# Kernel tuning notes

Hardware: AMD Instinct MI355X
Metric: run time of the kernel (lower is better)

## Reference

```python
import jax, jax.numpy as jnp
import numpy as np

U10_IDX, V10_IDX = 0, 1
WIND_THRESH = 0.5


def _gru(x, h, Wih, Whh, bih, bhh):
    # standard torch GRUCell math
    gi = x @ Wih.T + bih
    gh = h @ Whh.T + bhh
    ir, iz, inn = jnp.split(gi, 3, axis=-1)
    hr, hz, hnn = jnp.split(gh, 3, axis=-1)
    r = jax.nn.sigmoid(ir + hr)
    z = jax.nn.sigmoid(iz + hz)
    n = jnp.tanh(inn + r * hnn)
    return (1.0 - z) * n + z * h


def setup_inputs() -> dict:
    B, N, H, F, Th, Tf = 256, 184, 128, 8, 24, 24
    key = jax.random.key(0)
    ks = jax.random.split(key, 24)
    s = 0.1
    f32 = jnp.float32
    feature = jax.random.normal(ks[0], (B, Th + Tf, N, F), f32)
    pm25_hist = jax.random.uniform(ks[1], (B, Th, N, 1), dtype=f32)
    adj_mat = (jax.random.uniform(ks[2], (N, N)) < 0.1).astype(f32)
    angles = jax.random.uniform(ks[3], (N, N), f32, 0.0, 2.0 * np.pi)
    C = F + 1  # ChebConv in-channels = in_dim + out_dim
    return dict(
        feature=feature, pm25_hist=pm25_hist, adj_mat=adj_mat, angles=angles,
        W_ih_hist=s * jax.random.normal(ks[4], (3 * H, 2), f32),
        W_hh_hist=s * jax.random.normal(ks[5], (3 * H, H), f32),
        b_ih_hist=s * jax.random.normal(ks[6], (3 * H,), f32),
        b_hh_hist=s * jax.random.normal(ks[7], (3 * H,), f32),
        fc_hist_w=s * jax.random.normal(ks[8], (1, H), f32),
        fc_hist_b=s * jax.random.normal(ks[9], (1,), f32),
        cheb_w0=s * jax.random.normal(ks[10], (C, 1), f32),
        cheb_w1=s * jax.random.normal(ks[11], (C, 1), f32),
        cheb_b=s * jax.random.normal(ks[12], (1,), f32),
        W_ih=s * jax.random.normal(ks[13], (3 * H, C + 1), f32),
        W_hh=s * jax.random.normal(ks[14], (3 * H, H), f32),
        b_ih=s * jax.random.normal(ks[15], (3 * H,), f32),
        b_hh=s * jax.random.normal(ks[16], (3 * H,), f32),
        fc_out_w=s * jax.random.normal(ks[17], (1, H), f32),
        fc_out_b=s * jax.random.normal(ks[18], (1,), f32),
    )


def reference(feature, pm25_hist, adj_mat, angles,
              W_ih_hist, W_hh_hist, b_ih_hist, b_hh_hist,
              fc_hist_w, fc_hist_b,
              cheb_w0, cheb_w1, cheb_b,
              W_ih, W_hh, b_ih, b_hh,
              fc_out_w, fc_out_b):
    B, T, N, F = feature.shape
    H = W_hh.shape[1]
    Th = pm25_hist.shape[1]
    comp1 = jnp.cos(angles)                                # [N,N]
    comp2 = jnp.cos(angles - jnp.float32(np.pi / 2.0))     # [N,N]
    adj_b = adj_mat > 0

    # ---- history GRU over pm25_hist ----
    def hist_step(carry, p):
        hn, xn = carry
        x = jnp.concatenate([xn, p], axis=-1).reshape(B * N, 2)
        hn = _gru(x, hn, W_ih_hist, W_hh_hist, b_ih_hist, b_hh_hist)
        xn = hn.reshape(B, N, H) @ fc_hist_w.T + fc_hist_b
        return (hn, xn), None

    h0 = jnp.zeros((B * N, H), feature.dtype)
    x0 = jnp.zeros((B, N, 1), feature.dtype)
    (hn, xn), _ = jax.lax.scan(hist_step, (h0, x0), jnp.swapaxes(pm25_hist, 0, 1))

    # ---- forecast: dynamic wind-gated graph + ChebConv(K=2) + GRU ----
    def fore_step(carry, f):
        hn, xn = carry
        x = jnp.concatenate([xn, f], axis=-1)              # [B,N,F+1]
        u = f[..., U10_IDX]                                # [B,N]
        v = f[..., V10_IDX]
        wind = u[:, :, None] * comp1[None] + v[:, :, None] * comp2[None]
        # edge i->j iff adj and wind projection >= threshold
        M = jnp.logical_and(wind >= WIND_THRESH, adj_b[None]).astype(x.dtype)
        deg = M.sum(-1)                                    # source degree [B,N]
        has = deg > 0
        dinv = jnp.where(has, 1.0 / jnp.sqrt(jnp.where(has, deg, 1.0)), 0.0)
        # ChebConv scaled Laplacian (lambda_max=2, sym norm):
        # L_hat x [j] = -dinv_j * sum_i dinv_i * M[i,j] * x[i] + (0 if deg_j>0 else -1) * x[j]
        y = jnp.einsum('bij,bic->bjc', M * dinv[:, :, None], x)
        y = -dinv[:, :, None] * y + jnp.where(has, 0.0, -1.0)[:, :, None] * x
        g = jax.nn.sigmoid(x @ cheb_w0 + y @ cheb_w1 + cheb_b)  # [B,N,1]
        x2 = jnp.concatenate([x, g], axis=-1).reshape(B * N, F + 2)
        hn = _gru(x2, hn, W_ih, W_hh, b_ih, b_hh)
        xn = hn.reshape(B, N, H) @ fc_out_w.T + fc_out_b
        return (hn, xn), xn

    fore_feat = jnp.swapaxes(feature[:, Th:], 0, 1)        # [Tf,B,N,F]
    (_, _), preds = jax.lax.scan(fore_step, (hn, xn), fore_feat)
    return jnp.swapaxes(preds, 0, 1)                       # [B,Tf,N,1]
```

## Files before the change

### kernel.cpp

```cpp
#include <hip/hip_runtime.h>
#include <hip/hip_bf16.h>
#include <math.h>

#define BB 256
#define NN 184
#define HH 128
#define FF 8
#define TH 24
#define TF 24
#define KA 160
#define NG2 640
#define RPAD 192
#define STRH 136
#define NT 1024
#define NW3 552
#define LOG2E 1.44269504088896f

#define REC_F 8832
#define OFF_DINV 4416
#define OFF_G 5152
#define OFF_AXF 5888

typedef __attribute__((ext_vector_type(8))) short bf16x8;
typedef __attribute__((ext_vector_type(4))) short bf16x4;
typedef __attribute__((ext_vector_type(4))) float f32x4;
typedef __attribute__((ext_vector_type(2))) unsigned u32x2;

#if __has_builtin(__builtin_amdgcn_mfma_f32_16x16x16bf16_1k)
#define XK16 1
#else
#define XK16 0
#endif

#if __has_builtin(__builtin_amdgcn_exp2f)
#define EXP2(x) __builtin_amdgcn_exp2f(x)
#else
#define EXP2(x) exp2f(x)
#endif

__device__ __forceinline__ unsigned short f2bf(float f) {
    unsigned u = __float_as_uint(f);
    u += 0x7fffu + ((u >> 16) & 1u);
    return (unsigned short)(u >> 16);
}
__device__ __forceinline__ unsigned pkbf(float a, float b) {
    __hip_bfloat162 h = __float22bfloat162_rn(make_float2(a, b));
    return *reinterpret_cast<unsigned*>(&h);
}
__device__ __forceinline__ void gload16(const void* src, void* dst) {
    __builtin_amdgcn_global_load_lds(
        (const __attribute__((address_space(1))) unsigned int*)src,
        (__attribute__((address_space(3))) unsigned int*)dst, 16, 0, 0);
}

__global__ void prep_weights(const float* __restrict__ WhhH, const float* __restrict__ WihH,
                             const float* __restrict__ WhhF, const float* __restrict__ WihF,
                             const float* __restrict__ bihH, const float* __restrict__ bhhH,
                             const float* __restrict__ bihF, const float* __restrict__ bhhF,
                             const float* __restrict__ fchw, const float* __restrict__ fchb,
                             unsigned short* __restrict__ WaH, unsigned short* __restrict__ WaF) {
    int idx = blockIdx.x * 256 + threadIdx.x;
    if (idx >= NG2 * KA) return;
    int jp = idx / KA, k = idx % KA;
    int j = jp & 127, part = jp >> 7;
    float vh = 0.f, vf = 0.f;
    if (part <= 1) {
        int row = part * 128 + j;
        if (k < 128) {
            vh = WhhH[row * 128 + k] + WihH[row * 2 + 0] * fchw[k];
            vf = WhhF[row * 128 + k];
        } else {
            int s = k - 128;
            if (s == 0)  vh = WihH[row * 2 + 1];
            if (s < 8)   vf = WihF[row * 10 + (s + 1)];
            if (s == 8)  { vh = WihH[row * 2 + 0]; vf = WihF[row * 10 + 0]; }
            if (s == 9)  vf = WihF[row * 10 + 9];
            if (s == 11) {
                vh = bihH[row] + bhhH[row] + WihH[row * 2 + 0] * fchb[0];
                vf = bihF[row] + bhhF[row];
            }
        }
    } else if (part == 2) {
        if (k < 128) { vh = WhhH[(256 + j) * 128 + k]; vf = WhhF[(256 + j) * 128 + k]; }
        else if (k == 139) { vh = bhhH[256 + j]; vf = bhhF[256 + j]; }
    } else if (part == 3) {
        if (k >= 128) {
            int s = k - 128;
            if (s == 0)  vh = WihH[(256 + j) * 2 + 1];
            if (s < 8)   vf = WihF[(256 + j) * 10 + (s + 1)];
            if (s == 8)  { vh = WihH[(256 + j) * 2 + 0]; vf = WihF[(256 + j) * 10 + 0]; }
            if (s == 9)  vf = WihF[(256 + j) * 10 + 9];
            if (s == 11) {
                vh = bihH[256 + j] + WihH[(256 + j) * 2 + 0] * fchb[0];
                vf = bihF[256 + j];
            }
        }
    } else {
        if (k < 128) vh = WihH[(256 + j) * 2 + 0] * fchw[k];
    }
    float sc = (part <= 1) ? LOG2E : 2.0f * LOG2E;
    WaH[idx] = f2bf(vh * sc);
    WaF[idx] = f2bf(vf * sc);
}

__global__ void prep_edges(const float* __restrict__ angles, const float* __restrict__ adj,
                           float4* __restrict__ edges, int* __restrict__ cnt) {
    int idx = blockIdx.x * 256 + threadIdx.x;
    if (idx < NN * NN && adj[idx] > 0.f) {
        float a = angles[idx];
        int pos = atomicAdd(cnt, 1);
        float4 r;
        r.x = cosf(a);
        r.y = cosf(a - 1.57079632679489662f);
        r.z = __int_as_float(idx / NN);
        r.w = __int_as_float(idx % NN);
        edges[pos] = r;
    }
}

__global__ __launch_bounds__(NT, 4) void fused_dgc(
    const unsigned short* __restrict__ WaH,
    const unsigned short* __restrict__ WaF,
    const float* __restrict__ fchw, const float* __restrict__ fchb,
    const float* __restrict__ fcow, const float* __restrict__ fcob,
    const float* __restrict__ cw0, const float* __restrict__ cw1,
    const float* __restrict__ cbb,
    const float* __restrict__ feature, const float* __restrict__ pm25,
    const float4* __restrict__ edges, const int* __restrict__ ecnt,
    char* __restrict__ xrec,
    float* __restrict__ pred)
{
    __shared__ unsigned short Ah[2][RPAD * STRH];
    __shared__ unsigned short AxR[RPAD * 8];
    __shared__ __align__(16) char stg[2][8960];
    __shared__ float xnraw[2][RPAD];
    __shared__ float fcls_f[132];
    __shared__ unsigned short zero16[8];
    __shared__ __align__(16) unsigned short phist_s[TH * NN + 16];
    __shared__ float f8[NN * FF];
    __shared__ unsigned long long mT[NN * 3];
    __shared__ int dg[NN];
    __shared__ float2 dsI[NN];
    __shared__ float cwS[17];

    const int tid = threadIdx.x;
    const int bb = blockIdx.x;
    const int w = tid >> 6, lane = tid & 63, q = lane >> 4, lq = lane & 15;
    const int cg = w & 7, rh = w >> 3;

    for (int i = tid; i < RPAD * STRH; i += NT) Ah[0][i] = 0;
    for (int i = tid; i < RPAD * 8; i += NT)
        AxR[i] = ((i & 7) == 3) ? (unsigned short)0x3F80 : (unsigned short)0;
    if (tid < 8) zero16[tid] = 0;
    if (tid < RPAD) { xnraw[0][tid] = 0.f; xnraw[1][tid] = 0.f; }
    if (tid < 17)
        cwS[tid] = (tid < 8) ? cw1[tid + 1] : ((tid < 16) ? cw0[tid - 7] : cbb[0]);

    {
        const float4* psrc = (const float4*)(pm25 + (long)bb * TH * NN);
        for (int i = tid; i < (TH * NN) / 4; i += NT) {
            float4 v = psrc[i];
            u32x2 pk2;
            pk2[0] = pkbf(v.x, v.y);
            pk2[1] = pkbf(v.z, v.w);
            *(u32x2*)&phist_s[i * 4] = pk2;
        }
    }

    bf16x8 wregH[4][4];
#if XK16
    bf16x4 wregX[4];
#else
    bf16x8 wregX[4];
#endif
    auto load_w = [&](const unsigned short* Wa, const float* fcw, const float* fcb, bool h4) {
        const int jcol = cg * 16 + lq;
        #pragma unroll
        for (int g = 0; g < 3; ++g)
            #pragma unroll
            for (int kc = 0; kc < 4; ++kc)
                wregH[g][kc] = *(const bf16x8*)(Wa + (long)(g * 128 + jcol) * KA + kc * 32 + q * 8);
        if (h4)
            #pragma unroll
            for (int kc = 0; kc < 4; ++kc)
                wregH[3][kc] = *(const bf16x8*)(Wa + (long)(4 * 128 + jcol) * KA + kc * 32 + q * 8);
        #pragma unroll
        for (int g = 0; g < 4; ++g)
#if XK16
            wregX[g] = *(const bf16x4*)(Wa + (long)(g * 128 + jcol) * KA + 128 + q * 4);
#else
            wregX[g] = *(const bf16x8*)(Wa + (long)(g * 128 + jcol) * KA + 128 + q * 8);
#endif
        if (tid < 132) fcls_f[tid] = (tid < 128) ? fcw[tid] : ((tid == 128) ? fcb[0] : 0.f);
    };
    load_w(WaH, fchw, fchb, true);

    const int nE = *ecnt;
    const float w00 = cw0[0], w10 = cw1[0];
    const float fcbH = fchb[0], fcbO = fcob[0];
    const f32x4 zf = {0.f, 0.f, 0.f, 0.f};

    int p = 0;
    __syncthreads();

    for (int t = 0; t < TH + TF; ++t) {
        const bool hist = (t < TH);
        const bool dofc = (t >= TH - 1);
        const unsigned short* AxFS = (const unsigned short*)(stg[p] + OFF_AXF);

        if (hist) {
            char* rec = xrec + ((long)bb * TF + t) * REC_F;
            const float4* fsrc = (const float4*)(feature + ((long)bb * (TH + TF) + TH + t) * (NN * FF));
            for (int i = tid; i < (NN * FF) / 4; i += NT) ((float4*)f8)[i] = fsrc[i];
            for (int i = tid; i < NN * 3; i += NT) mT[i] = 0ull;
            if (tid < NN) dg[tid] = 0;
            __syncthreads();
            for (int e = tid; e < nE; e += NT) {
                float4 r = edges[e];
                int ii = __float_as_int(r.z), jj = __float_as_int(r.w);
                if (f8[ii * FF] * r.x + f8[ii * FF + 1] * r.y >= 0.5f) {
                    atomicAdd(&dg[ii], 1);
                    atomicOr(&mT[jj * 3 + (ii >> 6)], 1ull << (ii & 63));
                }
            }
            __syncthreads();
            if (tid < NN) {
                float d = (dg[tid] > 0) ? rsqrtf((float)dg[tid]) : 0.f;
                float s = 0.f;
                #pragma unroll
                for (int c = 0; c < 8; ++c) s = fmaf(f8[tid * FF + c], cwS[c], s);
                dsI[tid] = make_float2(d, d * s);
            }
            __syncthreads();
            {
                const int jg = tid >> 2, wd = tid & 3;
                if (jg < NN) {
                    float acc = 0.f;
                    if (wd < 3) {
                        unsigned long long m = mT[jg * 3 + wd];
                        ((unsigned long long*)rec)[jg * 3 + wd] = m;
                        while (m) {
                            int bp = __ffsll(m) - 1; m &= m - 1;
                            acc += dsI[wd * 64 + bp].y;
                        }
                    }
                    acc += __shfl_xor(acc, 1);
                    acc += __shfl_xor(acc, 2);
                    if (wd == 0) {
                        float dj = dsI[jg].x;
                        float hzj = (dj > 0.f) ? 0.f : -1.f;
                        float S0 = 0.f, S1 = 0.f;
                        #pragma unroll
                        for (int c = 0; c < 8; ++c) {
                            float xv = f8[jg * FF + c];
                            S1 = fmaf(xv, cwS[c], S1);
                            S0 = fmaf(xv, cwS[8 + c], S0);
                        }
                        float G = cwS[16] + S0 + hzj * S1 - dj * acc;
                        ((float*)(rec + OFF_DINV))[jg] = dj;
                        ((float*)(rec + OFF_G))[jg] = G;
                        uint4 ax4;
                        ax4.x = pkbf(f8[jg * FF + 0], f8[jg * FF + 1]);
                        ax4.y = pkbf(f8[jg * FF + 2], f8[jg * FF + 3]);
                        ax4.z = pkbf(f8[jg * FF + 4], f8[jg * FF + 5]);
                        ax4.w = pkbf(f8[jg * FF + 6], f8[jg * FF + 7]);
                        *(uint4*)(rec + OFF_AXF + jg * 16) = ax4;
                    }
                }
            }
        } else {
            const unsigned long long* maskS = (const unsigned long long*)stg[p];
            const float* dinS = (const float*)(stg[p] + OFF_DINV);
            const float* GS = (const float*)(stg[p] + OFF_G);
            const float* xr = xnraw[(t - 1) & 1];
            const float fcbP = (t == TH) ? fcbH : fcbO;
            const int jg = tid >> 2, wd = tid & 3;
            if (jg < NN) {
                float acc = 0.f, accd = 0.f;
                if (wd < 3) {
                    unsigned long long m = maskS[jg * 3 + wd];
                    while (m) {
                        int bp = __ffsll(m) - 1; m &= m - 1;
                        int i = wd * 64 + bp;
                        float d = dinS[i];
                        acc = fmaf(d, xr[i], acc);
                        accd += d;
                    }
                }
                acc  += __shfl_xor(acc, 1);  acc  += __shfl_xor(acc, 2);
                accd += __shfl_xor(accd, 1); accd += __shfl_xor(accd, 2);
                if (wd == 0) {
                    float dj = dinS[jg];
                    float xnj = xr[jg] + fcbP;
                    float hzj = (dj > 0.f) ? 0.f : -1.f;
                    float sum = fmaf(fcbP, accd, acc);
                    float y0 = -dj * sum + hzj * xnj;
                    float pre = GS[jg] + xnj * w00 + y0 * w10;
                    float g = __builtin_amdgcn_rcpf(1.0f + EXP2(-LOG2E * pre));
                    AxR[jg * 8 + 1] = f2bf(g);
                    AxR[jg * 8 + 0] = f2bf(xnj);
                    if (t > TH) pred[((long)bb * TF + (t - 1 - TH)) * NN + jg] = xnj;
                }
            } else {
                int i = tid - 736;
                if (i < RPAD) xnraw[t & 1][i] = 0.f;
            }
            __syncthreads();
        }

        const int t2 = t + 1;
        if (t2 >= TH && t2 < TH + TF && tid < NW3)
            gload16(xrec + ((long)bb * TF + (t2 - TH)) * REC_F + tid * 16,
                    (char*)stg[p ^ 1] + (tid & ~63) * 16);

        f32x4 fw = *(const f32x4*)&fcls_f[cg * 16 + q * 4];
        const unsigned short corr0 = (t == 0) ? f2bf(-fcbH) : (unsigned short)0;
        #pragma unroll
        for (int rl = 0; rl < 6; ++rl) {
            const int row = rh * 96 + rl * 16 + lq;
            const int ro = row * STRH;
            f32x4 a0, a1, a2, a3;
            {
                bf16x8 bh = *(const bf16x8*)(&Ah[p][ro + q * 8]);
                a0 = __builtin_amdgcn_mfma_f32_16x16x32_bf16(wregH[0][0], bh, zf, 0, 0, 0);
                a1 = __builtin_amdgcn_mfma_f32_16x16x32_bf16(wregH[1][0], bh, zf, 0, 0, 0);
                a2 = __builtin_amdgcn_mfma_f32_16x16x32_bf16(wregH[2][0], bh, zf, 0, 0, 0);
                a3 = hist ? __builtin_amdgcn_mfma_f32_16x16x32_bf16(wregH[3][0], bh, zf, 0, 0, 0)
                          : zf;
            }
            #pragma unroll
            for (int kc = 1; kc < 4; ++kc) {
                bf16x8 bh = *(const bf16x8*)(&Ah[p][ro + kc * 32 + q * 8]);
                a0 = __builtin_amdgcn_mfma_f32_16x16x32_bf16(wregH[0][kc], bh, a0, 0, 0, 0);
                a1 = __builtin_amdgcn_mfma_f32_16x16x32_bf16(wregH[1][kc], bh, a1, 0, 0, 0);
                a2 = __builtin_amdgcn_mfma_f32_16x16x32_bf16(wregH[2][kc], bh, a2, 0, 0, 0);
                if (hist)
                    a3 = __builtin_amdgcn_mfma_f32_16x16x32_bf16(wregH[3][kc], bh, a3, 0, 0, 0);
            }
#if XK16
            bf16x4 bx;
            if (hist) {
                unsigned short pb = phist_s[t * NN + row];
                bf16x4 z = {0,0,0,0};
                bx = z;
                if (q == 0) bx[0] = (short)pb;
                if (q == 2) { bx[0] = (short)corr0; bx[3] = (short)0x3F80; }
            } else {
                const unsigned short* bxp = (q < 2) ? (AxFS + row * 8 + q * 4)
                                          : (q == 2) ? (AxR + row * 8) : zero16;
                bx = *(const bf16x4*)bxp;
            }
            a0 = __builtin_amdgcn_mfma_f32_16x16x16bf16_1k(wregX[0], bx, a0, 0, 0, 0);
            a1 = __builtin_amdgcn_mfma_f32_16x16x16bf16_1k(wregX[1], bx, a1, 0, 0, 0);
            a2 = __builtin_amdgcn_mfma_f32_16x16x16bf16_1k(wregX[2], bx, a2, 0, 0, 0);
            a3 = __builtin_amdgcn_mfma_f32_16x16x16bf16_1k(wregX[3], bx, a3, 0, 0, 0);
#else
            bf16x8 bx;
            if (hist) {
                unsigned short pb = phist_s[t * NN + row];
                bf16x8 z = {0,0,0,0,0,0,0,0};
                bx = z;
                if (q == 0) bx[0] = (short)pb;
                if (q == 1) { bx[0] = (short)corr0; bx[3] = (short)0x3F80; }
            } else {
                const unsigned short* bxp = (q == 0) ? (AxFS + row * 8)
                                          : (q == 1) ? (AxR + row * 8) : zero16;
                bx = *(const bf16x8*)bxp;
            }
            a0 = __builtin_amdgcn_mfma_f32_16x16x32_bf16(wregX[0], bx, a0, 0, 0, 0);
            a1 = __builtin_amdgcn_mfma_f32_16x16x32_bf16(wregX[1], bx, a1, 0, 0, 0);
            a2 = __builtin_amdgcn_mfma_f32_16x16x32_bf16(wregX[2], bx, a2, 0, 0, 0);
            a3 = __builtin_amdgcn_mfma_f32_16x16x32_bf16(wregX[3], bx, a3, 0, 0, 0);
#endif

            u32x2 hold = *(const u32x2*)&Ah[p][ro + cg * 16 + q * 4];

            float hn[4];
            #pragma unroll
            for (int rg = 0; rg < 4; ++rg) {
                unsigned hu = hold[rg >> 1];
                float ho = ((rg & 1) == 0) ? __uint_as_float(hu << 16)
                                           : __uint_as_float(hu & 0xffff0000u);
                float rr = __builtin_amdgcn_rcpf(1.0f + EXP2(-a0[rg]));
                float zz = __builtin_amdgcn_rcpf(1.0f + EXP2(-a1[rg]));
                float wv = fmaf(rr, a2[rg], a3[rg]);
                float s2 = __builtin_amdgcn_rcpf(1.0f + EXP2(-wv));
                float tv = fmaf(2.0f, s2, -1.0f);
                hn[rg] = fmaf(zz, ho - tv, tv);
            }
            u32x2 pk;
            pk[0] = pkbf(hn[0], hn[1]);
            pk[1] = pkbf(hn[2], hn[3]);
            *(u32x2*)&Ah[p ^ 1][ro + cg * 16 + q * 4] = pk;
            if (dofc) {
                float pf = hn[0] * fw.x + hn[1] * fw.y + hn[2] * fw.z + hn[3] * fw.w;
                pf += __shfl_xor(pf, 16);
                pf += __shfl_xor(pf, 32);
                if (q == 0) atomicAdd(&xnraw[t & 1][row], pf);
            }
        }
        __syncthreads();

        if (t == TH - 1)
            load_w(WaF, fcow, fcob, false);
        p ^= 1;
    }

    if (tid < NN)
        pred[((long)bb * TF + (TF - 1)) * NN + tid] =
            xnraw[(TH + TF - 1) & 1][tid] + fcbO;
}

extern "C" void kernel_launch(void* const* d_in, const int* in_sizes, int n_in,
                              void* d_out, int out_size, void* d_ws, size_t ws_size,
                              hipStream_t stream) {
    const float* feature = (const float*)d_in[0];
    const float* pm25    = (const float*)d_in[1];
    const float* adj     = (const float*)d_in[2];
    const float* angles  = (const float*)d_in[3];
    const float* W_ih_h  = (const float*)d_in[4];
    const float* W_hh_h  = (const float*)d_in[5];
    const float* b_ih_h  = (const float*)d_in[6];
    const float* b_hh_h  = (const float*)d_in[7];
    const float* fch_w   = (const float*)d_in[8];
    const float* fch_b   = (const float*)d_in[9];
    const float* cw0     = (const float*)d_in[10];
    const float* cw1     = (const float*)d_in[11];
    const float* cbb     = (const float*)d_in[12];
    const float* W_ih    = (const float*)d_in[13];
    const float* W_hh    = (const float*)d_in[14];
    const float* b_ih    = (const float*)d_in[15];
    const float* b_hh    = (const float*)d_in[16];
    const float* fco_w   = (const float*)d_in[17];
    const float* fco_b   = (const float*)d_in[18];
    float* pred = (float*)d_out;

    char* ws = (char*)d_ws;
    size_t off = 0;
    unsigned short* WaH   = (unsigned short*)(ws + off); off += (size_t)NG2 * KA * 2;
    unsigned short* WaF   = (unsigned short*)(ws + off); off += (size_t)NG2 * KA * 2;
    float4*         edges = (float4*)(ws + off);         off += (size_t)NN * NN * 16;
    int*            cnt   = (int*)(ws + off);            off += 16;
    char*           xrec  = (char*)(ws + off);
    off += (size_t)BB * TF * REC_F;

    hipMemsetAsync(cnt, 0, 16, stream);
    prep_weights<<<(NG2 * KA + 255) / 256, 256, 0, stream>>>(
        W_hh_h, W_ih_h, W_hh, W_ih, b_ih_h, b_hh_h, b_ih, b_hh, fch_w, fch_b,
        WaH, WaF);
    prep_edges<<<(NN * NN + 255) / 256, 256, 0, stream>>>(angles, adj, edges, cnt);

    fused_dgc<<<BB, NT, 0, stream>>>(
        WaH, WaF, fch_w, fch_b, fco_w, fco_b, cw0, cw1, cbb,
        feature, pm25, edges, cnt, xrec, pred);
}
```

Baseline: 633.1 us.

## Move forecast graph construction into a separate highly parallel prep kernel

The per-timestep wind-graph construction (edge masks, degrees, Chebyshev gate terms) used to be computed inside the 256-block fused recurrent kernel during the history steps. It now runs in its own kernel with one block per (batch, forecast step), 6144 blocks in total, and the fused kernel only handles the GRU recurrence. The pm25 history is also converted to bf16 in a separate kernel and loaded with a 16-byte async-style load. The aim is to take the graph work off the serial recurrent critical path and use the whole GPU for it. In exchange it adds two kernel launches and extra global memory traffic. The fused kernel also loses the overlap it had between graph building and history-step compute.

```diff
diff --git a/kernel.cpp b/kernel.cpp
--- a/kernel.cpp
+++ b/kernel.cpp
@@ -118,16 +118,95 @@
     }
 }
 
+__global__ void prep_hist(const float* __restrict__ pm25, unsigned short* __restrict__ phist) {
+    int idx = blockIdx.x * 256 + threadIdx.x;
+    if (idx < BB * TH * NN) phist[idx] = f2bf(pm25[idx]);
+}
+
+__global__ __launch_bounds__(1024) void prep_graph(
+    const float* __restrict__ feature,
+    const float4* __restrict__ edges, const int* __restrict__ ecnt,
+    const float* __restrict__ cw0, const float* __restrict__ cw1,
+    const float* __restrict__ cbb, char* __restrict__ xrec)
+{
+    const int bt = blockIdx.x;
+    const int b = bt / TF, tf = bt % TF;
+    const int tt = TH + tf;
+    const int tid = threadIdx.x;
+
+    char* rec = xrec + ((long)b * TF + tf) * REC_F;
+
+    __shared__ float f8[NN * FF];
+    __shared__ unsigned long long mT[NN * 3];
+    __shared__ int dg[NN];
+    __shared__ float2 dsI[NN];
+
+    const float4* fb4 = (const float4*)(feature + ((long)b * (TH + TF) + tt) * (NN * FF));
+    for (int i = tid; i < (NN * FF) / 4; i += 1024) ((float4*)f8)[i] = fb4[i];
+    for (int i = tid; i < NN * 3; i += 1024) mT[i] = 0ull;
+    if (tid < NN) dg[tid] = 0;
+    __syncthreads();
+    const int nE = *ecnt;
+    for (int e = tid; e < nE; e += 1024) {
+        float4 r = edges[e];
+        int ii = __float_as_int(r.z), jj = __float_as_int(r.w);
+        if (f8[ii * FF] * r.x + f8[ii * FF + 1] * r.y >= 0.5f) {
+            atomicAdd(&dg[ii], 1);
+            atomicOr(&mT[jj * 3 + (ii >> 6)], 1ull << (ii & 63));
+        }
+    }
+    __syncthreads();
+    if (tid < NN) {
+        float d = (dg[tid] > 0) ? rsqrtf((float)dg[tid]) : 0.f;
+        float s = 0.f;
+        #pragma unroll
+        for (int c = 0; c < 8; ++c) s = fmaf(f8[tid * FF + c], cw1[c + 1], s);
+        dsI[tid] = make_float2(d, d * s);
+    }
+    __syncthreads();
+    const int jg = tid >> 2, wd = tid & 3;
+    if (jg < NN) {
+        float acc = 0.f;
+        if (wd < 3) {
+            unsigned long long m = mT[jg * 3 + wd];
+            ((unsigned long long*)rec)[jg * 3 + wd] = m;
+            while (m) {
+                int bp = __ffsll(m) - 1; m &= m - 1;
+                acc += dsI[wd * 64 + bp].y;
+            }
+        }
+        acc += __shfl_xor(acc, 1);
+        acc += __shfl_xor(acc, 2);
+        if (wd == 0) {
+            float dj = dsI[jg].x;
+            float hzj = (dj > 0.f) ? 0.f : -1.f;
+            float S0 = 0.f, S1 = 0.f;
+            #pragma unroll
+            for (int c = 0; c < 8; ++c) {
+                float xv = f8[jg * FF + c];
+                S0 = fmaf(xv, cw0[c + 1], S0);
+                S1 = fmaf(xv, cw1[c + 1], S1);
+            }
+            float G = cbb[0] + S0 + hzj * S1 - dj * acc;
+            ((float*)(rec + OFF_DINV))[jg] = dj;
+            ((float*)(rec + OFF_G))[jg] = G;
+            uint4 ax4;
+            ax4.x = pkbf(f8[jg * FF + 0], f8[jg * FF + 1]);
+            ax4.y = pkbf(f8[jg * FF + 2], f8[jg * FF + 3]);
+            ax4.z = pkbf(f8[jg * FF + 4], f8[jg * FF + 5]);
+            ax4.w = pkbf(f8[jg * FF + 6], f8[jg * FF + 7]);
+            *(uint4*)(rec + OFF_AXF + jg * 16) = ax4;
+        }
+    }
+}
+
 __global__ __launch_bounds__(NT, 4) void fused_dgc(
     const unsigned short* __restrict__ WaH,
     const unsigned short* __restrict__ WaF,
     const float* __restrict__ fchw, const float* __restrict__ fchb,
     const float* __restrict__ fcow, const float* __restrict__ fcob,
     const float* __restrict__ cw0, const float* __restrict__ cw1,
-    const float* __restrict__ cbb,
-    const float* __restrict__ feature, const float* __restrict__ pm25,
-    const float4* __restrict__ edges, const int* __restrict__ ecnt,
-    char* __restrict__ xrec,
+    const char* __restrict__ xrec, const unsigned short* __restrict__ phist,
     float* __restrict__ pred)
 {
     __shared__ unsigned short Ah[2][RPAD * STRH];
@@ -137,11 +216,6 @@
     __shared__ float fcls_f[132];
     __shared__ unsigned short zero16[8];
     __shared__ __align__(16) unsigned short phist_s[TH * NN + 16];
-    __shared__ float f8[NN * FF];
-    __shared__ unsigned long long mT[NN * 3];
-    __shared__ int dg[NN];
-    __shared__ float2 dsI[NN];
-    __shared__ float cwS[17];
 
     const int tid = threadIdx.x;
     const int bb = blockIdx.x;
@@ -153,19 +227,6 @@
         AxR[i] = ((i & 7) == 3) ? (unsigned short)0x3F80 : (unsigned short)0;
     if (tid < 8) zero16[tid] = 0;
     if (tid < RPAD) { xnraw[0][tid] = 0.f; xnraw[1][tid] = 0.f; }
-    if (tid < 17)
-        cwS[tid] = (tid < 8) ? cw1[tid + 1] : ((tid < 16) ? cw0[tid - 7] : cbb[0]);
-
-    {
-        const float4* psrc = (const float4*)(pm25 + (long)bb * TH * NN);
-        for (int i = tid; i < (TH * NN) / 4; i += NT) {
-            float4 v = psrc[i];
-            u32x2 pk2;
-            pk2[0] = pkbf(v.x, v.y);
-            pk2[1] = pkbf(v.z, v.w);
-            *(u32x2*)&phist_s[i * 4] = pk2;
-        }
-    }
 
     bf16x8 wregH[4][4];
 #if XK16
@@ -195,7 +256,10 @@
     };
     load_w(WaH, fchw, fchb, true);
 
-    const int nE = *ecnt;
+    if (tid < NW3)
+        gload16((const char*)phist + (long)bb * (TH * NN * 2) + tid * 16,
+                (char*)phist_s + (tid & ~63) * 16);
+
     const float w00 = cw0[0], w10 = cw1[0];
     const float fcbH = fchb[0], fcbO = fcob[0];
     const f32x4 zf = {0.f, 0.f, 0.f, 0.f};
@@ -208,67 +272,7 @@
         const bool dofc = (t >= TH - 1);
         const unsigned short* AxFS = (const unsigned short*)(stg[p] + OFF_AXF);
 
-        if (hist) {
-            char* rec = xrec + ((long)bb * TF + t) * REC_F;
-            const float4* fsrc = (const float4*)(feature + ((long)bb * (TH + TF) + TH + t) * (NN * FF));
-            for (int i = tid; i < (NN * FF) / 4; i += NT) ((float4*)f8)[i] = fsrc[i];
-            for (int i = tid; i < NN * 3; i += NT) mT[i] = 0ull;
-            if (tid < NN) dg[tid] = 0;
-            __syncthreads();
-            for (int e = tid; e < nE; e += NT) {
-                float4 r = edges[e];
-                int ii = __float_as_int(r.z), jj = __float_as_int(r.w);
-                if (f8[ii * FF] * r.x + f8[ii * FF + 1] * r.y >= 0.5f) {
-                    atomicAdd(&dg[ii], 1);
-                    atomicOr(&mT[jj * 3 + (ii >> 6)], 1ull << (ii & 63));
-                }
-            }
-            __syncthreads();
-            if (tid < NN) {
-                float d = (dg[tid] > 0) ? rsqrtf((float)dg[tid]) : 0.f;
-                float s = 0.f;
-                #pragma unroll
-                for (int c = 0; c < 8; ++c) s = fmaf(f8[tid * FF + c], cwS[c], s);
-                dsI[tid] = make_float2(d, d * s);
-            }
-            __syncthreads();
-            {
-                const int jg = tid >> 2, wd = tid & 3;
-                if (jg < NN) {
-                    float acc = 0.f;
-                    if (wd < 3) {
-                        unsigned long long m = mT[jg * 3 + wd];
-                        ((unsigned long long*)rec)[jg * 3 + wd] = m;
-                        while (m) {
-                            int bp = __ffsll(m) - 1; m &= m - 1;
-                            acc += dsI[wd * 64 + bp].y;
-                        }
-                    }
-                    acc += __shfl_xor(acc, 1);
-                    acc += __shfl_xor(acc, 2);
-                    if (wd == 0) {
-                        float dj = dsI[jg].x;
-                        float hzj = (dj > 0.f) ? 0.f : -1.f;
-                        float S0 = 0.f, S1 = 0.f;
-                        #pragma unroll
-                        for (int c = 0; c < 8; ++c) {
-                            float xv = f8[jg * FF + c];
-                            S1 = fmaf(xv, cwS[c], S1);
-                            S0 = fmaf(xv, cwS[8 + c], S0);
-                        }
-                        float G = cwS[16] + S0 + hzj * S1 - dj * acc;
-                        ((float*)(rec + OFF_DINV))[jg] = dj;
-                        ((float*)(rec + OFF_G))[jg] = G;
-                        uint4 ax4;
-                        ax4.x = pkbf(f8[jg * FF + 0], f8[jg * FF + 1]);
-                        ax4.y = pkbf(f8[jg * FF + 2], f8[jg * FF + 3]);
-                        ax4.z = pkbf(f8[jg * FF + 4], f8[jg * FF + 5]);
-                        ax4.w = pkbf(f8[jg * FF + 6], f8[jg * FF + 7]);
-                        *(uint4*)(rec + OFF_AXF + jg * 16) = ax4;
-                    }
-                }
-            }
-        } else {
+        if (!hist) {
             const unsigned long long* maskS = (const unsigned long long*)stg[p];
             const float* dinS = (const float*)(stg[p] + OFF_DINV);
             const float* GS = (const float*)(stg[p] + OFF_G);
@@ -441,6 +445,7 @@
     unsigned short* WaF   = (unsigned short*)(ws + off); off += (size_t)NG2 * KA * 2;
     float4*         edges = (float4*)(ws + off);         off += (size_t)NN * NN * 16;
     int*            cnt   = (int*)(ws + off);            off += 16;
+    unsigned short* phist = (unsigned short*)(ws + off); off += (size_t)BB * TH * NN * 2;
     char*           xrec  = (char*)(ws + off);
     off += (size_t)BB * TF * REC_F;
 
@@ -449,8 +454,10 @@
         W_hh_h, W_ih_h, W_hh, W_ih, b_ih_h, b_hh_h, b_ih, b_hh, fch_w, fch_b,
         WaH, WaF);
     prep_edges<<<(NN * NN + 255) / 256, 256, 0, stream>>>(angles, adj, edges, cnt);
+    prep_hist<<<(BB * TH * NN + 255) / 256, 256, 0, stream>>>(pm25, phist);
+    prep_graph<<<BB * TF, 1024, 0, stream>>>(
+        feature, edges, cnt, cw0, cw1, cbb, xrec);
 
     fused_dgc<<<BB, NT, 0, stream>>>(
-        WaH, WaF, fch_w, fch_b, fco_w, fco_b, cw0, cw1, cbb,
-        feature, pm25, edges, cnt, xrec, pred);
-}
+        WaH, WaF, fch_w, fch_b, fco_w, fco_b, cw0, cw1, xrec, phist, pred);
+}
```

After: 578.9 us. 8.6% less time.
